# Kernel tuning notes

Hardware: AMD Instinct MI355X
Metric: run time of the kernel (lower is better)

Reference implementation:

```python
import jax, jax.numpy as jnp
import numpy as np
from jax import lax

NUM_HEADS = 8
EPS_BN = 1e-5
EPS_LN = 1e-5


def setup_inputs() -> dict:
    key = jax.random.key(0)
    ks = iter(jax.random.split(key, 32))
    C = 512
    R = C // 16  # channel-gate reduction
    HID = 512    # classifier hidden
    NC = 1       # num_classes

    def gn(shape, scale=0.02):
        return (jax.random.normal(next(ks), shape, dtype=jnp.float32) * scale)

    inp = {
        "x": jax.random.normal(next(ks), (16, C, 28, 28), dtype=jnp.float32),
        # ChannelGate MLP (Linear(C,R) -> ReLU -> Linear(R,C))
        "mlp_w1": gn((R, C)), "mlp_b1": jnp.zeros((R,), jnp.float32),
        "mlp_w2": gn((C, R)), "mlp_b2": jnp.zeros((C,), jnp.float32),
        # SpatialGate 7x7 conv (2->1, no bias) + BatchNorm2d(1) eval-mode stats
        "sp_w": gn((1, 2, 7, 7)),
        "sp_gamma": jnp.ones((1,), jnp.float32), "sp_beta": jnp.zeros((1,), jnp.float32),
        "sp_mean": jnp.zeros((1,), jnp.float32), "sp_var": jnp.ones((1,), jnp.float32),
        # attention projections
        "wq": gn((C, C)), "bq": jnp.zeros((C,), jnp.float32),
        "wk": gn((C, C)), "bk": jnp.zeros((C,), jnp.float32),
        "wv": gn((C, C)), "bv": jnp.zeros((C,), jnp.float32),
        "wo": gn((C, C)), "bo": jnp.zeros((C,), jnp.float32),
        # classifier: LayerNorm(C) -> Linear(C,512) -> ReLU -> Linear(512,NC)
        "ln_g": jnp.ones((C,), jnp.float32), "ln_b": jnp.zeros((C,), jnp.float32),
        "fc1_w": gn((HID, C)), "fc1_b": jnp.zeros((HID,), jnp.float32),
        "fc2_w": gn((NC, HID)), "fc2_b": jnp.zeros((NC,), jnp.float32),
    }
    return inp


def reference(x, mlp_w1, mlp_b1, mlp_w2, mlp_b2, sp_w, sp_gamma, sp_beta,
              sp_mean, sp_var, wq, bq, wk, bk, wv, bv, wo, bo,
              ln_g, ln_b, fc1_w, fc1_b, fc2_w, fc2_b):
    B, C, H, W = x.shape
    N = H * W
    hd = C // NUM_HEADS

    # ---- CBAM: channel gate (avg + max global pools through shared MLP) ----
    def mlp(p):  # p: [B, C]
        return jax.nn.relu(p @ mlp_w1.T + mlp_b1) @ mlp_w2.T + mlp_b2

    avg_p = x.mean(axis=(2, 3))
    max_p = x.max(axis=(2, 3))
    ch_scale = jax.nn.sigmoid(mlp(avg_p) + mlp(max_p))[:, :, None, None]
    x = x * ch_scale

    # ---- CBAM: spatial gate ----
    comp = jnp.concatenate([x.max(axis=1, keepdims=True),
                            x.mean(axis=1, keepdims=True)], axis=1)  # [B,2,H,W]
    s = lax.conv_general_dilated(comp, sp_w, window_strides=(1, 1),
                                 padding=[(3, 3), (3, 3)],
                                 dimension_numbers=("NCHW", "OIHW", "NCHW"))
    s = (s - sp_mean[None, :, None, None]) * lax.rsqrt(sp_var + EPS_BN)[None, :, None, None]
    s = s * sp_gamma[None, :, None, None] + sp_beta[None, :, None, None]
    x = x * jax.nn.sigmoid(s)

    # ---- multi-head self-attention over HW tokens ----
    xf = x.reshape(B, C, N).transpose(0, 2, 1)  # [B, N, C]

    def heads(w, b):
        return (xf @ w.T + b).reshape(B, N, NUM_HEADS, hd).transpose(0, 2, 1, 3)

    Q, K, V = heads(wq, bq), heads(wk, bk), heads(wv, bv)  # [B, h, N, d]
    scores = jnp.einsum("bhnd,bhmd->bhnm", Q, K) / jnp.sqrt(jnp.float32(hd))
    attn = jax.nn.softmax(scores, axis=-1)  # dropout is identity in eval
    attended = jnp.einsum("bhnm,bhmd->bhnd", attn, V)
    attended = attended.transpose(0, 2, 1, 3).reshape(B, N, C)
    attended = attended @ wo.T + bo
    x = x + attended.transpose(0, 2, 1).reshape(B, C, H, W)

    # ---- classifier head ----
    p = x.mean(axis=(2, 3))  # AdaptiveAvgPool2d(1) + Flatten -> [B, C]
    mu = p.mean(axis=-1, keepdims=True)
    var = p.var(axis=-1, keepdims=True)
    ln = (p - mu) * lax.rsqrt(var + EPS_LN) * ln_g + ln_b
    h = jax.nn.relu(ln @ fc1_w.T + fc1_b)
    return h @ fc2_w.T + fc2_b
```

## Files before the change

### kernel.cpp

```cpp
#include <hip/hip_runtime.h>
#include <math.h>

#define BB 16
#define CC 512
#define HW 784
#define RR 32
#define NHD 8
#define HD 64
#define NT 784
#define NTILE 49
#define CBS 132

#define OFS_AVGP   0
#define OFS_MAXP   8192
#define OFS_CHS    16384
#define OFS_SP     49664
#define OFS_P1     62208
#define OFS_ABAR   70400
#define OFS_XG     78592
#define XG_SZ      (BB*CC*HW)
#define OFS_XGT    (OFS_XG + XG_SZ)
#define OFS_QBF    (OFS_XGT + XG_SZ/2)
#define OFS_KBF    (OFS_QBF + XG_SZ/2)
#define OFS_V2     (OFS_KBF + XG_SZ/2)
#define OFS_WF     (OFS_V2 + XG_SZ)
#define OFS_W      OFS_XG
#define OFS_PV     (OFS_XG + 131072)
#define OFS_H1     (OFS_PV + 8192)
#define OFS_CMAXP  (OFS_XG + 262144)
#define OFS_CMEANP (OFS_CMAXP + 200704)

typedef __attribute__((ext_vector_type(8))) short bf16x8;
typedef __attribute__((ext_vector_type(4))) float f32x4;

__device__ __forceinline__ unsigned short f2bf(float x) {
  union { float f; unsigned u; } v; v.f = x;
  unsigned r = v.u + 0x7fffu + ((v.u >> 16) & 1u);
  return (unsigned short)(r >> 16);
}
__device__ __forceinline__ float bf2f(unsigned short x) {
  union { unsigned u; float f; } v; v.u = ((unsigned)x) << 16;
  return v.f;
}
__device__ __forceinline__ void async16(const unsigned short* g, unsigned short* l) {
  __builtin_amdgcn_global_load_lds(
      (const __attribute__((address_space(1))) unsigned int*)g,
      (__attribute__((address_space(3))) unsigned int*)l, 16, 0, 0);
}

__global__ void k_pool(const float* __restrict__ x, float* avg_p, float* max_p) {
  int wid = threadIdx.x >> 6;
  int lane = threadIdx.x & 63;
  int row = blockIdx.x * 4 + wid;
  const float* xr = x + (size_t)row * HW;
  float s = 0.f, m = -INFINITY;
  for (int i = lane; i < HW; i += 64) { float v = xr[i]; s += v; m = fmaxf(m, v); }
  for (int o = 32; o; o >>= 1) { s += __shfl_down(s, o, 64); m = fmaxf(m, __shfl_down(m, o, 64)); }
  if (lane == 0) { avg_p[row] = s * (1.f/HW); max_p[row] = m; }
}

__global__ void k_chmlp(const float* avg_p, const float* max_p,
                        const float* w1, const float* b1,
                        const float* w2, const float* b2, float* chs) {
  __shared__ float pa[CC], pm[CC], part[256], hr[64];
  int b = blockIdx.x, t = threadIdx.x;
  for (int i = t; i < CC; i += 256) { pa[i] = avg_p[b*CC+i]; pm[i] = max_p[b*CC+i]; }
  __syncthreads();
  {
    int rp = t & 63, ch = t >> 6;
    int r = rp & 31;
    const float* src = (rp < 32) ? pa : pm;
    const float* wr = w1 + (size_t)r*CC + ch*128;
    float s = 0.f;
    #pragma unroll 8
    for (int c = 0; c < 128; c++) s += src[ch*128 + c] * wr[c];
    part[t] = s;
  }
  __syncthreads();
  if (t < 64)
    hr[t] = fmaxf(part[t] + part[64+t] + part[128+t] + part[192+t] + b1[t & 31], 0.f);
  __syncthreads();
  for (int c = t; c < CC; c += 256) {
    float a = 2.f*b2[c];
    const float* wr = w2 + c*RR;
    #pragma unroll
    for (int r = 0; r < RR; r++) a += (hr[r]+hr[32+r])*wr[r];
    chs[b*CC+c] = 1.f/(1.f+__expf(-a));
  }
}

__global__ void k_chgatep(const float* __restrict__ x, const float* __restrict__ chs,
                          float* __restrict__ cmaxp, float* __restrict__ cmeanp) {
  __shared__ float cs[32];
  int b = blockIdx.x, cg = blockIdx.y, t = threadIdx.x;
  if (t < 32) cs[t] = chs[b*CC + cg*32 + t];
  __syncthreads();
  const float* xb = x + ((size_t)b*CC + cg*32)*HW;
  for (int pix = t; pix < HW; pix += 256) {
    float mx = -INFINITY, sm = 0.f;
    #pragma unroll
    for (int c = 0; c < 32; c++) {
      float v = xb[(size_t)c*HW + pix] * cs[c];
      mx = fmaxf(mx, v); sm += v;
    }
    cmaxp[(size_t)(cg*BB + b)*HW + pix] = mx;
    cmeanp[(size_t)(cg*BB + b)*HW + pix] = sm;
  }
}

__global__ void k_credsp(const float* __restrict__ cmaxp, const float* __restrict__ cmeanp,
                         const float* __restrict__ w, const float* g, const float* be,
                         const float* mu, const float* var, float* __restrict__ sp) {
  __shared__ float cmx[HW], cmn[HW];
  int b = blockIdx.x, t = threadIdx.x;
  for (int pix = t; pix < HW; pix += 256) {
    float mx = -INFINITY, sm = 0.f;
    #pragma unroll
    for (int cg = 0; cg < 16; cg++) {
      mx = fmaxf(mx, cmaxp[(size_t)(cg*BB + b)*HW + pix]);
      sm += cmeanp[(size_t)(cg*BB + b)*HW + pix];
    }
    cmx[pix] = mx; cmn[pix] = sm * (1.f/CC);
  }
  __syncthreads();
  float bnscale = rsqrtf(var[0]+1e-5f)*g[0];
  for (int pix = t; pix < HW; pix += 256) {
    int h = pix/28, wd = pix%28;
    float acc = 0.f;
    for (int kh = 0; kh < 7; kh++) {
      int ih = h + kh - 3; if (ih < 0 || ih >= 28) continue;
      for (int kw = 0; kw < 7; kw++) {
        int iw = wd + kw - 3; if (iw < 0 || iw >= 28) continue;
        int ip = ih*28+iw;
        acc += cmx[ip]*w[kh*7+kw] + cmn[ip]*w[49+kh*7+kw];
      }
    }
    float s = (acc - mu[0])*bnscale + be[0];
    sp[b*HW+pix] = 1.f/(1.f+__expf(-s));
  }
}

__global__ void k_sfuse(const float* __restrict__ x, const float* __restrict__ chs,
                        const float* __restrict__ sp, unsigned short* __restrict__ xgT) {
  __shared__ float cs[CC];
  int nt = blockIdx.x, b = blockIdx.y;
  int t = threadIdx.x, ln = t & 63;
  for (int i = t; i < CC; i += 256) cs[i] = chs[b*CC+i];
  __syncthreads();
  int n = nt*16 + (ln & 15);
  float spv = sp[b*HW + n];
  const float* xb = x + (size_t)b*CC*HW;
  #pragma unroll
  for (int i = 0; i < 4; i++) {
    int s = (t >> 6) + 4*i;
    int c = s*32 + (ln >> 4)*8;
    bf16x8 p;
    #pragma unroll
    for (int j = 0; j < 8; j++)
      p[j] = (short)f2bf(xb[(size_t)(c+j)*HW + n] * cs[c+j] * spv);
    *(bf16x8*)(xgT + ((((size_t)b*NTILE + nt)*16 + s)*64 + ln)*8) = p;
  }
}

__global__ void k_p1(const unsigned short* __restrict__ xgT, float* __restrict__ p1) {
  __shared__ float red[4][32];
  int b = blockIdx.x, s = blockIdx.y;
  int t = threadIdx.x, w = t >> 6, ln = t & 63;
  float acc[8] = {0.f,0.f,0.f,0.f,0.f,0.f,0.f,0.f};
  for (int nt = w; nt < NTILE; nt += 4) {
    bf16x8 p = *(const bf16x8*)(xgT + ((((size_t)b*NTILE + nt)*16 + s)*64 + ln)*8);
    #pragma unroll
    for (int j = 0; j < 8; j++) acc[j] += bf2f((unsigned short)p[j]);
  }
  #pragma unroll
  for (int j = 0; j < 8; j++) {
    float v = acc[j];
    v += __shfl_xor(v,1,64); v += __shfl_xor(v,2,64);
    v += __shfl_xor(v,4,64); v += __shfl_xor(v,8,64);
    if ((ln & 15) == 0) red[w][(ln>>4)*8 + j] = v;
  }
  __syncthreads();
  if (t < 32)
    p1[b*CC + s*32 + t] = (red[0][t]+red[1][t]+red[2][t]+red[3][t]) * (1.f/HW);
}

__global__ void k_wfrag(const float* __restrict__ wq, const float* __restrict__ wk,
                        const float* __restrict__ wv, unsigned short* __restrict__ Wf) {
  int idx = blockIdx.x*256 + threadIdx.x;
  int ln = idx & 63;
  int s  = (idx >> 6) & 15;
  int ct = (idx >> 10) & 31;
  int mat = idx >> 15;
  const float* W = (mat==0)? wq : (mat==1)? wk : wv;
  const float* src = W + (size_t)(ct*16 + (ln & 15))*CC + s*32 + (ln >> 4)*8;
  float4 f0 = *(const float4*)src;
  float4 f1 = *(const float4*)(src + 4);
  bf16x8 p;
  p[0]=(short)f2bf(f0.x); p[1]=(short)f2bf(f0.y); p[2]=(short)f2bf(f0.z); p[3]=(short)f2bf(f0.w);
  p[4]=(short)f2bf(f1.x); p[5]=(short)f2bf(f1.y); p[6]=(short)f2bf(f1.z); p[7]=(short)f2bf(f1.w);
  *(bf16x8*)(Wf + (size_t)idx*8) = p;
}

__global__ __launch_bounds__(256) void k_qkv_mfma(
    const unsigned short* __restrict__ xgT, const unsigned short* __restrict__ Wf,
    const float* __restrict__ bq, const float* __restrict__ bk, const float* __restrict__ bv,
    unsigned short* __restrict__ Qbf, unsigned short* __restrict__ Kbf,
    unsigned short* __restrict__ Vbf) {
  __shared__ __align__(16) unsigned char smem[65536];
  unsigned short* Alds = (unsigned short*)smem;
  float* Cb = (float*)smem;
  int blk = blockIdx.x;
  int yb = blk / 208;
  int r0 = blk % 208;
  int mt = r0 >> 4;
  int b  = r0 & 15;
  int mat = yb >> 2;
  int c0 = (yb & 3) * 128;
  int t = threadIdx.x, w = t >> 6, ln = t & 63;
  const unsigned short* Ab = xgT + (size_t)b*NTILE*8192;
  const unsigned short* Bb = Wf + (size_t)mat*32*8192;
  int ctg0 = (c0 >> 4) + w*2;
  int ntc[4];
  #pragma unroll
  for (int m = 0; m < 4; m++) { int nt = 4*mt + m; ntc[m] = (nt > 48) ? 48 : nt; }
  #pragma unroll
  for (int j0 = 0; j0 < 16; j0++) {
    int j = w + 4*j0;
    int m = j >> 4, sj = j & 15;
    async16(Ab + (size_t)ntc[m]*8192 + (size_t)(sj*64 + ln)*8,
            Alds + (size_t)j*512);
  }
  f32x4 acc[4][2];
  #pragma unroll
  for (int m = 0; m < 4; m++)
    #pragma unroll
    for (int c2 = 0; c2 < 2; c2++) acc[m][c2] = (f32x4){0.f,0.f,0.f,0.f};
  __syncthreads();
  #pragma unroll 2
  for (int s = 0; s < 16; s++) {
    bf16x8 bf0 = *(const bf16x8*)(Bb + (size_t)(ctg0*16 + s)*512 + ln*8);
    bf16x8 bf1 = *(const bf16x8*)(Bb + (size_t)((ctg0+1)*16 + s)*512 + ln*8);
    bf16x8 af[4];
    #pragma unroll
    for (int m = 0; m < 4; m++)
      af[m] = *(const bf16x8*)(Alds + (size_t)(m*16 + s)*512 + ln*8);
    #pragma unroll
    for (int m = 0; m < 4; m++) {
      acc[m][0] = __builtin_amdgcn_mfma_f32_16x16x32_bf16(af[m], bf0, acc[m][0], 0,0,0);
      acc[m][1] = __builtin_amdgcn_mfma_f32_16x16x32_bf16(af[m], bf1, acc[m][1], 0,0,0);
    }
  }
  __syncthreads();
  #pragma unroll
  for (int m = 0; m < 4; m++)
    #pragma unroll
    for (int c2 = 0; c2 < 2; c2++)
      #pragma unroll
      for (int r = 0; r < 4; r++)
        Cb[(m*16 + (ln>>4)*4 + r)*CBS + w*32 + c2*16 + (ln&15)] = acc[m][c2][r];
  __syncthreads();
  const float* bias = (mat==0)? bq : (mat==1)? bk : bv;
  #pragma unroll
  for (int i = 0; i < 4; i++) {
    int p = w*4 + i;
    int ntl = p >> 2, sl = p & 3;
    int nt = 4*mt + ntl;
    if (nt > 48) continue;
    int row = ntl*16 + (ln & 15);
    int col = sl*32 + (ln >> 4)*8;
    float4 v0 = *(const float4*)&Cb[row*CBS + col];
    float4 v1 = *(const float4*)&Cb[row*CBS + col + 4];
    float v[8] = {v0.x, v0.y, v0.z, v0.w, v1.x, v1.y, v1.z, v1.w};
    #pragma unroll
    for (int j = 0; j < 8; j++) v[j] += bias[c0 + col + j];
    int token = nt*16 + (ln & 15);
    int h = (c0 >> 6) + (sl >> 1);
    int bh = b*NHD + h;
    bf16x8 pk;
    #pragma unroll
    for (int j = 0; j < 8; j++) pk[j] = (short)f2bf(v[j]);
    if (mat < 2) {
      unsigned short* Out = (mat == 0) ? Qbf : Kbf;
      *(bf16x8*)(Out + ((size_t)bh*NTILE + nt)*1024 + (size_t)(sl & 1)*512 + ln*8) = pk;
    } else {
      int d = (sl & 1)*32 + (ln >> 4)*8;
      *(bf16x8*)(Vbf + ((size_t)bh*NT + token)*HD + d) = pk;
    }
  }
}

__global__ __launch_bounds__(256, 3) void k_attn8(const unsigned short* __restrict__ Qbf,
    const unsigned short* __restrict__ Kbf, float* __restrict__ wsum) {
  __shared__ float l_tmp[2][64];
  __shared__ float rl[2][16];
  int bh = blockIdx.x & 127, pg = blockIdx.x >> 7;
  int t = threadIdx.x, w = t >> 6, ln = t & 63;
  int ntA = pg*2;
  bool hasB = (ntA + 1) < NTILE;
  int ntB = hasB ? (ntA + 1) : ntA;
  const unsigned short* QbA = Qbf + ((size_t)bh*NTILE + ntA)*1024;
  const unsigned short* QbB = Qbf + ((size_t)bh*NTILE + ntB)*1024;
  const unsigned short* Kb = Kbf + (size_t)bh*NTILE*1024;
  bf16x8 qA0 = *(const bf16x8*)(QbA + ln*8);
  bf16x8 qA1 = *(const bf16x8*)(QbA + 512 + ln*8);
  bf16x8 qB0 = *(const bf16x8*)(QbB + ln*8);
  bf16x8 qB1 = *(const bf16x8*)(QbB + 512 + ln*8);
  f32x4 evA[13], evB[13];
  float lpA[4] = {0.f,0.f,0.f,0.f}, lpB[4] = {0.f,0.f,0.f,0.f};
  #pragma unroll
  for (int i = 0; i < 13; i++) {
    int mt = w + 4*i;
    bool valid = (i < 12) || (w == 0);
    int mtc = valid ? mt : 48;
    bf16x8 k0 = *(const bf16x8*)(Kb + (size_t)mtc*1024 + ln*8);
    bf16x8 k1 = *(const bf16x8*)(Kb + (size_t)mtc*1024 + 512 + ln*8);
    f32x4 a = {0.f,0.f,0.f,0.f};
    a = __builtin_amdgcn_mfma_f32_16x16x32_bf16(qA0, k0, a, 0,0,0);
    a = __builtin_amdgcn_mfma_f32_16x16x32_bf16(qA1, k1, a, 0,0,0);
    f32x4 c = {0.f,0.f,0.f,0.f};
    c = __builtin_amdgcn_mfma_f32_16x16x32_bf16(qB0, k0, c, 0,0,0);
    c = __builtin_amdgcn_mfma_f32_16x16x32_bf16(qB1, k1, c, 0,0,0);
    f32x4 ea, eb;
    #pragma unroll
    for (int r = 0; r < 4; r++) {
      ea[r] = __expf(a[r]*0.125f);
      eb[r] = __expf(c[r]*0.125f);
    }
    evA[i] = ea; evB[i] = eb;
    if (valid) {
      #pragma unroll
      for (int r = 0; r < 4; r++) { lpA[r] += ea[r]; lpB[r] += eb[r]; }
    }
  }
  #pragma unroll
  for (int r = 0; r < 4; r++) {
    float v = lpA[r];
    v += __shfl_xor(v,1,64); v += __shfl_xor(v,2,64);
    v += __shfl_xor(v,4,64); v += __shfl_xor(v,8,64);
    if ((ln & 15) == 0) l_tmp[0][w*16 + (ln>>4)*4 + r] = v;
    float u = lpB[r];
    u += __shfl_xor(u,1,64); u += __shfl_xor(u,2,64);
    u += __shfl_xor(u,4,64); u += __shfl_xor(u,8,64);
    if ((ln & 15) == 0) l_tmp[1][w*16 + (ln>>4)*4 + r] = u;
  }
  __syncthreads();
  if (t < 32) {
    int g = t >> 4, q = t & 15;
    rl[g][q] = 1.f / (l_tmp[g][q] + l_tmp[g][16+q] + l_tmp[g][32+q] + l_tmp[g][48+q]);
  }
  __syncthreads();
  f32x4 rlA = *(const f32x4*)&rl[0][(ln >> 4)*4];
  f32x4 rlB = *(const f32x4*)&rl[1][(ln >> 4)*4];
  #pragma unroll
  for (int i = 0; i < 13; i++) {
    int mt = w + 4*i;
    bool valid = (i < 12) || (w == 0);
    float v = evA[i][0]*rlA[0] + evA[i][1]*rlA[1] + evA[i][2]*rlA[2] + evA[i][3]*rlA[3];
    if (hasB)
      v += evB[i][0]*rlB[0] + evB[i][1]*rlB[1] + evB[i][2]*rlB[2] + evB[i][3]*rlB[3];
    v += __shfl_xor(v, 16, 64);
    v += __shfl_xor(v, 32, 64);
    if (valid && ln < 16)
      atomicAdd(&wsum[bh*NT + mt*16 + ln], v);
  }
}

__global__ void k_attn_av(const float* __restrict__ w, const unsigned short* __restrict__ Vm,
                          float* __restrict__ abar) {
  __shared__ float red[256];
  int bh = blockIdx.x, t = threadIdx.x;
  int d = t & 63, chunk = t >> 6;
  float acc = 0.f;
  const unsigned short* vb = Vm + (size_t)bh*NT*HD;
  const float* wb = w + bh*NT;
  for (int m = chunk*196; m < (chunk+1)*196; m++)
    acc += wb[m] * bf2f(vb[(size_t)m*HD + d]);
  red[t] = acc;
  __syncthreads();
  if (t < 64)
    abar[bh*HD + t] = (red[t] + red[64+t] + red[128+t] + red[192+t]) * (1.f/NT);
}

__global__ void k_headA(const float* __restrict__ p1, const float* __restrict__ abar,
                        const float* __restrict__ wo, const float* __restrict__ bo,
                        float* __restrict__ pv) {
  int b = blockIdx.x, cg = blockIdx.y;
  int t = threadIdx.x, w = t >> 6, ln = t & 63;
  float a[8];
  #pragma unroll
  for (int k = 0; k < 8; k++) a[k] = abar[b*CC + ln + 64*k];
  int c0 = cg*32 + w*8;
  for (int i = 0; i < 8; i++) {
    int c = c0 + i;
    const float* wr = wo + (size_t)c*CC;
    float s = 0.f;
    #pragma unroll
    for (int k = 0; k < 8; k++) s += a[k] * wr[ln + 64*k];
    for (int o = 32; o; o >>= 1) s += __shfl_down(s, o, 64);
    if (ln == 0) pv[b*CC + c] = s + bo[c] + p1[b*CC + c];
  }
}

__global__ void k_headC(const float* __restrict__ pv, const float* __restrict__ ln_g,
                        const float* __restrict__ ln_b, const float* __restrict__ fc1_w,
                        const float* __restrict__ fc1_b, const float* __restrict__ fc2_w,
                        const float* __restrict__ fc2_b, float* __restrict__ out) {
  int b = blockIdx.x, cg = blockIdx.y;
  int t = threadIdx.x, w = t >> 6, ln = t & 63;
  float a[8];
  float s = 0.f, s2 = 0.f;
  #pragma unroll
  for (int k = 0; k < 8; k++) {
    a[k] = pv[b*CC + ln + 64*k];
    s += a[k]; s2 += a[k]*a[k];
  }
  for (int o = 32; o; o >>= 1) { s += __shfl_down(s, o, 64); s2 += __shfl_down(s2, o, 64); }
  s = __shfl(s, 0, 64); s2 = __shfl(s2, 0, 64);
  float mean = s * (1.f/CC);
  float rs = rsqrtf(s2*(1.f/CC) - mean*mean + 1e-5f);
  #pragma unroll
  for (int k = 0; k < 8; k++)
    a[k] = (a[k]-mean)*rs*ln_g[ln + 64*k] + ln_b[ln + 64*k];
  int c0 = cg*32 + w*8;
  float o2 = 0.f;
  for (int i = 0; i < 8; i++) {
    int c = c0 + i;
    const float* wr = fc1_w + (size_t)c*CC;
    float v = 0.f;
    #pragma unroll
    for (int k = 0; k < 8; k++) v += a[k] * wr[ln + 64*k];
    for (int o = 32; o; o >>= 1) v += __shfl_down(v, o, 64);
    if (ln == 0) o2 += fmaxf(v + fc1_b[c], 0.f) * fc2_w[c];
  }
  if (ln == 0) {
    if (cg == 0 && w == 0) o2 += fc2_b[0];
    atomicAdd(&out[b], o2);
  }
}

extern "C" void kernel_launch(void* const* d_in, const int* in_sizes, int n_in,
                              void* d_out, int out_size, void* d_ws, size_t ws_size,
                              hipStream_t stream) {
  const float* x       = (const float*)d_in[0];
  const float* mlp_w1  = (const float*)d_in[1];
  const float* mlp_b1  = (const float*)d_in[2];
  const float* mlp_w2  = (const float*)d_in[3];
  const float* mlp_b2  = (const float*)d_in[4];
  const float* sp_w    = (const float*)d_in[5];
  const float* sp_g    = (const float*)d_in[6];
  const float* sp_b    = (const float*)d_in[7];
  const float* sp_mu   = (const float*)d_in[8];
  const float* sp_var  = (const float*)d_in[9];
  const float* wq      = (const float*)d_in[10];
  const float* bq      = (const float*)d_in[11];
  const float* wk      = (const float*)d_in[12];
  const float* bk      = (const float*)d_in[13];
  const float* wv      = (const float*)d_in[14];
  const float* bv      = (const float*)d_in[15];
  const float* wo      = (const float*)d_in[16];
  const float* bo      = (const float*)d_in[17];
  const float* ln_g    = (const float*)d_in[18];
  const float* ln_b    = (const float*)d_in[19];
  const float* fc1_w   = (const float*)d_in[20];
  const float* fc1_b   = (const float*)d_in[21];
  const float* fc2_w   = (const float*)d_in[22];
  const float* fc2_b   = (const float*)d_in[23];

  float* ws = (float*)d_ws;
  float* avg_p = ws + OFS_AVGP;
  float* max_p = ws + OFS_MAXP;
  float* chs   = ws + OFS_CHS;
  float* sp    = ws + OFS_SP;
  float* p1    = ws + OFS_P1;
  float* abar  = ws + OFS_ABAR;
  unsigned short* xgT = (unsigned short*)(ws + OFS_XGT);
  unsigned short* Qbf = (unsigned short*)(ws + OFS_QBF);
  unsigned short* Kbf = (unsigned short*)(ws + OFS_KBF);
  unsigned short* Vbf = (unsigned short*)(ws + OFS_V2);
  unsigned short* Wf  = (unsigned short*)(ws + OFS_WF);
  float* wsum  = ws + OFS_W;
  float* pv    = ws + OFS_PV;
  float* cmaxp = ws + OFS_CMAXP;
  float* cmeanp= ws + OFS_CMEANP;

  hipMemsetAsync(wsum, 0, BB*NHD*NT*sizeof(float), stream);
  hipMemsetAsync(d_out, 0, (size_t)out_size*sizeof(float), stream);

  k_pool   <<<2048, 256, 0, stream>>>(x, avg_p, max_p);
  k_chmlp  <<<BB, 256, 0, stream>>>(avg_p, max_p, mlp_w1, mlp_b1, mlp_w2, mlp_b2, chs);
  k_chgatep<<<dim3(BB,16), 256, 0, stream>>>(x, chs, cmaxp, cmeanp);
  k_credsp <<<BB, 256, 0, stream>>>(cmaxp, cmeanp, sp_w, sp_g, sp_b, sp_mu, sp_var, sp);
  k_wfrag  <<<384, 256, 0, stream>>>(wq, wk, wv, Wf);
  k_sfuse  <<<dim3(NTILE,BB), 256, 0, stream>>>(x, chs, sp, xgT);
  k_p1     <<<dim3(BB,16), 256, 0, stream>>>(xgT, p1);
  k_qkv_mfma<<<2496, 256, 0, stream>>>(xgT, Wf, bq, bk, bv, Qbf, Kbf, Vbf);
  k_attn8  <<<25*128, 256, 0, stream>>>(Qbf, Kbf, wsum);
  k_attn_av<<<128, 256, 0, stream>>>(wsum, Vbf, abar);
  k_headA  <<<dim3(BB,16), 256, 0, stream>>>(p1, abar, wo, bo, pv);
  k_headC  <<<dim3(BB,16), 256, 0, stream>>>(pv, ln_g, ln_b, fc1_w, fc1_b,
                                             fc2_w, fc2_b, (float*)d_out);
}
```

Before: 270.5 us.

## Fuse prologue, pooling and head kernels; widen QKV tile to 256 columns

Merges the pooling, weight-fragment conversion and workspace zeroing into one launch, which removes the two memsets. The p1 channel mean is folded into the spatial-fuse kernel via shuffle reductions and atomics, computed from fp32 values instead of rereading the bf16 output. The attention-average, output projection, LayerNorm and classifier are fused into a single 512-thread kernel per batch. The QKV MFMA kernel now computes 256 columns per block, halving its grid and reusing each A tile more. The spatial conv is split across four blocks per batch. This cuts launch count and global round trips, at the cost of a very small, serial head kernel (16 blocks) and more float atomics.

Measured after the change: 350.2 us. +29.5%, slower.

```diff
diff --git a/kernel.cpp b/kernel.cpp
--- a/kernel.cpp
+++ b/kernel.cpp
@@ -25,8 +25,6 @@
 #define OFS_V2     (OFS_KBF + XG_SZ/2)
 #define OFS_WF     (OFS_V2 + XG_SZ)
 #define OFS_W      OFS_XG
-#define OFS_PV     (OFS_XG + 131072)
-#define OFS_H1     (OFS_PV + 8192)
 #define OFS_CMAXP  (OFS_XG + 262144)
 #define OFS_CMEANP (OFS_CMAXP + 200704)
 
@@ -48,15 +46,43 @@
       (__attribute__((address_space(3))) unsigned int*)l, 16, 0, 0);
 }
 
-__global__ void k_pool(const float* __restrict__ x, float* avg_p, float* max_p) {
-  int wid = threadIdx.x >> 6;
-  int lane = threadIdx.x & 63;
-  int row = blockIdx.x * 4 + wid;
-  const float* xr = x + (size_t)row * HW;
-  float s = 0.f, m = -INFINITY;
-  for (int i = lane; i < HW; i += 64) { float v = xr[i]; s += v; m = fmaxf(m, v); }
-  for (int o = 32; o; o >>= 1) { s += __shfl_down(s, o, 64); m = fmaxf(m, __shfl_down(m, o, 64)); }
-  if (lane == 0) { avg_p[row] = s * (1.f/HW); max_p[row] = m; }
+__global__ void k_pre(const float* __restrict__ x,
+                      const float* __restrict__ wq, const float* __restrict__ wk,
+                      const float* __restrict__ wv,
+                      float* avg_p, float* max_p, unsigned short* __restrict__ Wf,
+                      float* __restrict__ wsum, float* __restrict__ p1) {
+  int bid = blockIdx.x;
+  if (bid < 2048) {
+    int wid = threadIdx.x >> 6;
+    int lane = threadIdx.x & 63;
+    int row = bid * 4 + wid;
+    const float* xr = x + (size_t)row * HW;
+    float s = 0.f, m = -INFINITY;
+    for (int i = lane; i < HW; i += 64) { float v = xr[i]; s += v; m = fmaxf(m, v); }
+    for (int o = 32; o; o >>= 1) { s += __shfl_down(s, o, 64); m = fmaxf(m, __shfl_down(m, o, 64)); }
+    if (lane == 0) { avg_p[row] = s * (1.f/HW); max_p[row] = m; }
+  } else if (bid < 2432) {
+    int idx = (bid - 2048)*256 + threadIdx.x;
+    int ln = idx & 63;
+    int s  = (idx >> 6) & 15;
+    int ct = (idx >> 10) & 31;
+    int mat = idx >> 15;
+    const float* W = (mat==0)? wq : (mat==1)? wk : wv;
+    const float* src = W + (size_t)(ct*16 + (ln & 15))*CC + s*32 + (ln >> 4)*8;
+    float4 f0 = *(const float4*)src;
+    float4 f1 = *(const float4*)(src + 4);
+    bf16x8 p;
+    p[0]=(short)f2bf(f0.x); p[1]=(short)f2bf(f0.y); p[2]=(short)f2bf(f0.z); p[3]=(short)f2bf(f0.w);
+    p[4]=(short)f2bf(f1.x); p[5]=(short)f2bf(f1.y); p[6]=(short)f2bf(f1.z); p[7]=(short)f2bf(f1.w);
+    *(bf16x8*)(Wf + (size_t)idx*8) = p;
+  } else {
+    int idx = (bid - 2432)*256 + threadIdx.x;
+    const float4 z = {0.f,0.f,0.f,0.f};
+    for (int i = idx; i < 27136; i += 16384) {
+      if (i < 25088) *(float4*)&wsum[(size_t)i*4] = z;
+      else           *(float4*)&p1[(size_t)(i-25088)*4] = z;
+    }
+  }
 }
 
 __global__ void k_chmlp(const float* avg_p, const float* max_p,
@@ -112,7 +138,7 @@
                          const float* __restrict__ w, const float* g, const float* be,
                          const float* mu, const float* var, float* __restrict__ sp) {
   __shared__ float cmx[HW], cmn[HW];
-  int b = blockIdx.x, t = threadIdx.x;
+  int b = blockIdx.x, q = blockIdx.y, t = threadIdx.x;
   for (int pix = t; pix < HW; pix += 256) {
     float mx = -INFINITY, sm = 0.f;
     #pragma unroll
@@ -123,8 +149,9 @@
     cmx[pix] = mx; cmn[pix] = sm * (1.f/CC);
   }
   __syncthreads();
-  float bnscale = rsqrtf(var[0]+1e-5f)*g[0];
-  for (int pix = t; pix < HW; pix += 256) {
+  if (t < 196) {
+    int pix = q*196 + t;
+    float bnscale = rsqrtf(var[0]+1e-5f)*g[0];
     int h = pix/28, wd = pix%28;
     float acc = 0.f;
     for (int kh = 0; kh < 7; kh++) {
@@ -141,7 +168,8 @@
 }
 
 __global__ void k_sfuse(const float* __restrict__ x, const float* __restrict__ chs,
-                        const float* __restrict__ sp, unsigned short* __restrict__ xgT) {
+                        const float* __restrict__ sp, unsigned short* __restrict__ xgT,
+                        float* __restrict__ p1) {
   __shared__ float cs[CC];
   int nt = blockIdx.x, b = blockIdx.y;
   int t = threadIdx.x, ln = t & 63;
@@ -154,51 +182,26 @@
   for (int i = 0; i < 4; i++) {
     int s = (t >> 6) + 4*i;
     int c = s*32 + (ln >> 4)*8;
+    float vf[8];
     bf16x8 p;
     #pragma unroll
-    for (int j = 0; j < 8; j++)
-      p[j] = (short)f2bf(xb[(size_t)(c+j)*HW + n] * cs[c+j] * spv);
+    for (int j = 0; j < 8; j++) {
+      vf[j] = xb[(size_t)(c+j)*HW + n] * cs[c+j] * spv;
+      p[j] = (short)f2bf(vf[j]);
+    }
     *(bf16x8*)(xgT + ((((size_t)b*NTILE + nt)*16 + s)*64 + ln)*8) = p;
-  }
-}
-
-__global__ void k_p1(const unsigned short* __restrict__ xgT, float* __restrict__ p1) {
-  __shared__ float red[4][32];
-  int b = blockIdx.x, s = blockIdx.y;
-  int t = threadIdx.x, w = t >> 6, ln = t & 63;
-  float acc[8] = {0.f,0.f,0.f,0.f,0.f,0.f,0.f,0.f};
-  for (int nt = w; nt < NTILE; nt += 4) {
-    bf16x8 p = *(const bf16x8*)(xgT + ((((size_t)b*NTILE + nt)*16 + s)*64 + ln)*8);
-    #pragma unroll
-    for (int j = 0; j < 8; j++) acc[j] += bf2f((unsigned short)p[j]);
-  }
-  #pragma unroll
-  for (int j = 0; j < 8; j++) {
-    float v = acc[j];
-    v += __shfl_xor(v,1,64); v += __shfl_xor(v,2,64);
-    v += __shfl_xor(v,4,64); v += __shfl_xor(v,8,64);
-    if ((ln & 15) == 0) red[w][(ln>>4)*8 + j] = v;
-  }
-  __syncthreads();
-  if (t < 32)
-    p1[b*CC + s*32 + t] = (red[0][t]+red[1][t]+red[2][t]+red[3][t]) * (1.f/HW);
-}
-
-__global__ void k_wfrag(const float* __restrict__ wq, const float* __restrict__ wk,
-                        const float* __restrict__ wv, unsigned short* __restrict__ Wf) {
-  int idx = blockIdx.x*256 + threadIdx.x;
-  int ln = idx & 63;
-  int s  = (idx >> 6) & 15;
-  int ct = (idx >> 10) & 31;
-  int mat = idx >> 15;
-  const float* W = (mat==0)? wq : (mat==1)? wk : wv;
-  const float* src = W + (size_t)(ct*16 + (ln & 15))*CC + s*32 + (ln >> 4)*8;
-  float4 f0 = *(const float4*)src;
-  float4 f1 = *(const float4*)(src + 4);
-  bf16x8 p;
-  p[0]=(short)f2bf(f0.x); p[1]=(short)f2bf(f0.y); p[2]=(short)f2bf(f0.z); p[3]=(short)f2bf(f0.w);
-  p[4]=(short)f2bf(f1.x); p[5]=(short)f2bf(f1.y); p[6]=(short)f2bf(f1.z); p[7]=(short)f2bf(f1.w);
-  *(bf16x8*)(Wf + (size_t)idx*8) = p;
+    #pragma unroll
+    for (int j = 0; j < 8; j++) {
+      float v = vf[j];
+      v += __shfl_xor(v,1,64); v += __shfl_xor(v,2,64);
+      v += __shfl_xor(v,4,64); v += __shfl_xor(v,8,64);
+      vf[j] = v;
+    }
+    if ((ln & 15) == 0) {
+      #pragma unroll
+      for (int j = 0; j < 8; j++) atomicAdd(&p1[b*CC + c + j], vf[j]);
+    }
+  }
 }
 
 __global__ __launch_bounds__(256) void k_qkv_mfma(
@@ -214,12 +217,12 @@
   int r0 = blk % 208;
   int mt = r0 >> 4;
   int b  = r0 & 15;
-  int mat = yb >> 2;
-  int c0 = (yb & 3) * 128;
+  int mat = yb >> 1;
+  int c0 = (yb & 1) * 256;
   int t = threadIdx.x, w = t >> 6, ln = t & 63;
   const unsigned short* Ab = xgT + (size_t)b*NTILE*8192;
   const unsigned short* Bb = Wf + (size_t)mat*32*8192;
-  int ctg0 = (c0 >> 4) + w*2;
+  int ctgb = (c0 >> 4) + w*2;
   int ntc[4];
   #pragma unroll
   for (int m = 0; m < 4; m++) { int nt = 4*mt + m; ntc[m] = (nt > 48) ? 48 : nt; }
@@ -230,61 +233,70 @@
     async16(Ab + (size_t)ntc[m]*8192 + (size_t)(sj*64 + ln)*8,
             Alds + (size_t)j*512);
   }
-  f32x4 acc[4][2];
+  f32x4 acc[4][4];
   #pragma unroll
   for (int m = 0; m < 4; m++)
     #pragma unroll
-    for (int c2 = 0; c2 < 2; c2++) acc[m][c2] = (f32x4){0.f,0.f,0.f,0.f};
+    for (int c2 = 0; c2 < 4; c2++) acc[m][c2] = (f32x4){0.f,0.f,0.f,0.f};
   __syncthreads();
   #pragma unroll 2
   for (int s = 0; s < 16; s++) {
-    bf16x8 bf0 = *(const bf16x8*)(Bb + (size_t)(ctg0*16 + s)*512 + ln*8);
-    bf16x8 bf1 = *(const bf16x8*)(Bb + (size_t)((ctg0+1)*16 + s)*512 + ln*8);
+    bf16x8 bf[4];
+    bf[0] = *(const bf16x8*)(Bb + (size_t)((ctgb  )*16 + s)*512 + ln*8);
+    bf[1] = *(const bf16x8*)(Bb + (size_t)((ctgb+1)*16 + s)*512 + ln*8);
+    bf[2] = *(const bf16x8*)(Bb + (size_t)((ctgb+8)*16 + s)*512 + ln*8);
+    bf[3] = *(const bf16x8*)(Bb + (size_t)((ctgb+9)*16 + s)*512 + ln*8);
     bf16x8 af[4];
     #pragma unroll
     for (int m = 0; m < 4; m++)
       af[m] = *(const bf16x8*)(Alds + (size_t)(m*16 + s)*512 + ln*8);
     #pragma unroll
     for (int m = 0; m < 4; m++) {
-      acc[m][0] = __builtin_amdgcn_mfma_f32_16x16x32_bf16(af[m], bf0, acc[m][0], 0,0,0);
-      acc[m][1] = __builtin_amdgcn_mfma_f32_16x16x32_bf16(af[m], bf1, acc[m][1], 0,0,0);
-    }
-  }
-  __syncthreads();
-  #pragma unroll
-  for (int m = 0; m < 4; m++)
-    #pragma unroll
-    for (int c2 = 0; c2 < 2; c2++)
-      #pragma unroll
-      for (int r = 0; r < 4; r++)
-        Cb[(m*16 + (ln>>4)*4 + r)*CBS + w*32 + c2*16 + (ln&15)] = acc[m][c2][r];
+      #pragma unroll
+      for (int c2 = 0; c2 < 4; c2++)
+        acc[m][c2] = __builtin_amdgcn_mfma_f32_16x16x32_bf16(af[m], bf[c2], acc[m][c2], 0,0,0);
+    }
+  }
   __syncthreads();
   const float* bias = (mat==0)? bq : (mat==1)? bk : bv;
   #pragma unroll
-  for (int i = 0; i < 4; i++) {
-    int p = w*4 + i;
-    int ntl = p >> 2, sl = p & 3;
-    int nt = 4*mt + ntl;
-    if (nt > 48) continue;
-    int row = ntl*16 + (ln & 15);
-    int col = sl*32 + (ln >> 4)*8;
-    float4 v0 = *(const float4*)&Cb[row*CBS + col];
-    float4 v1 = *(const float4*)&Cb[row*CBS + col + 4];
-    float v[8] = {v0.x, v0.y, v0.z, v0.w, v1.x, v1.y, v1.z, v1.w};
-    #pragma unroll
-    for (int j = 0; j < 8; j++) v[j] += bias[c0 + col + j];
-    int token = nt*16 + (ln & 15);
-    int h = (c0 >> 6) + (sl >> 1);
-    int bh = b*NHD + h;
-    bf16x8 pk;
-    #pragma unroll
-    for (int j = 0; j < 8; j++) pk[j] = (short)f2bf(v[j]);
-    if (mat < 2) {
-      unsigned short* Out = (mat == 0) ? Qbf : Kbf;
-      *(bf16x8*)(Out + ((size_t)bh*NTILE + nt)*1024 + (size_t)(sl & 1)*512 + ln*8) = pk;
-    } else {
-      int d = (sl & 1)*32 + (ln >> 4)*8;
-      *(bf16x8*)(Vbf + ((size_t)bh*NT + token)*HD + d) = pk;
+  for (int ch = 0; ch < 2; ch++) {
+    if (ch) __syncthreads();
+    #pragma unroll
+    for (int m = 0; m < 4; m++)
+      #pragma unroll
+      for (int c2 = 0; c2 < 2; c2++)
+        #pragma unroll
+        for (int r = 0; r < 4; r++)
+          Cb[(m*16 + (ln>>4)*4 + r)*CBS + w*32 + c2*16 + (ln&15)] = acc[m][ch*2+c2][r];
+    __syncthreads();
+    #pragma unroll
+    for (int i = 0; i < 4; i++) {
+      int p = w*4 + i;
+      int ntl = p >> 2, sl = p & 3;
+      int nt = 4*mt + ntl;
+      if (nt > 48) continue;
+      int row = ntl*16 + (ln & 15);
+      int col = sl*32 + (ln >> 4)*8;
+      float4 v0 = *(const float4*)&Cb[row*CBS + col];
+      float4 v1 = *(const float4*)&Cb[row*CBS + col + 4];
+      float v[8] = {v0.x, v0.y, v0.z, v0.w, v1.x, v1.y, v1.z, v1.w};
+      int colA = ch*128 + col;
+      #pragma unroll
+      for (int j = 0; j < 8; j++) v[j] += bias[c0 + colA + j];
+      int token = nt*16 + (ln & 15);
+      int h = (c0 >> 6) + (ch << 1) + (sl >> 1);
+      int bh = b*NHD + h;
+      bf16x8 pk;
+      #pragma unroll
+      for (int j = 0; j < 8; j++) pk[j] = (short)f2bf(v[j]);
+      if (mat < 2) {
+        unsigned short* Out = (mat == 0) ? Qbf : Kbf;
+        *(bf16x8*)(Out + ((size_t)bh*NTILE + nt)*1024 + (size_t)(sl & 1)*512 + ln*8) = pk;
+      } else {
+        int d = (sl & 1)*32 + (ln >> 4)*8;
+        *(bf16x8*)(Vbf + ((size_t)bh*NT + token)*HD + d) = pk;
+      }
     }
   }
 }
@@ -365,76 +377,81 @@
   }
 }
 
-__global__ void k_attn_av(const float* __restrict__ w, const unsigned short* __restrict__ Vm,
-                          float* __restrict__ abar) {
-  __shared__ float red[256];
-  int bh = blockIdx.x, t = threadIdx.x;
-  int d = t & 63, chunk = t >> 6;
-  float acc = 0.f;
-  const unsigned short* vb = Vm + (size_t)bh*NT*HD;
-  const float* wb = w + bh*NT;
-  for (int m = chunk*196; m < (chunk+1)*196; m++)
-    acc += wb[m] * bf2f(vb[(size_t)m*HD + d]);
-  red[t] = acc;
-  __syncthreads();
-  if (t < 64)
-    abar[bh*HD + t] = (red[t] + red[64+t] + red[128+t] + red[192+t]) * (1.f/NT);
-}
-
-__global__ void k_headA(const float* __restrict__ p1, const float* __restrict__ abar,
-                        const float* __restrict__ wo, const float* __restrict__ bo,
-                        float* __restrict__ pv) {
-  int b = blockIdx.x, cg = blockIdx.y;
-  int t = threadIdx.x, w = t >> 6, ln = t & 63;
-  float a[8];
-  #pragma unroll
-  for (int k = 0; k < 8; k++) a[k] = abar[b*CC + ln + 64*k];
-  int c0 = cg*32 + w*8;
-  for (int i = 0; i < 8; i++) {
-    int c = c0 + i;
-    const float* wr = wo + (size_t)c*CC;
-    float s = 0.f;
-    #pragma unroll
-    for (int k = 0; k < 8; k++) s += a[k] * wr[ln + 64*k];
-    for (int o = 32; o; o >>= 1) s += __shfl_down(s, o, 64);
-    if (ln == 0) pv[b*CC + c] = s + bo[c] + p1[b*CC + c];
-  }
-}
-
-__global__ void k_headC(const float* __restrict__ pv, const float* __restrict__ ln_g,
-                        const float* __restrict__ ln_b, const float* __restrict__ fc1_w,
-                        const float* __restrict__ fc1_b, const float* __restrict__ fc2_w,
-                        const float* __restrict__ fc2_b, float* __restrict__ out) {
-  int b = blockIdx.x, cg = blockIdx.y;
-  int t = threadIdx.x, w = t >> 6, ln = t & 63;
-  float a[8];
-  float s = 0.f, s2 = 0.f;
-  #pragma unroll
-  for (int k = 0; k < 8; k++) {
-    a[k] = pv[b*CC + ln + 64*k];
-    s += a[k]; s2 += a[k]*a[k];
-  }
-  for (int o = 32; o; o >>= 1) { s += __shfl_down(s, o, 64); s2 += __shfl_down(s2, o, 64); }
-  s = __shfl(s, 0, 64); s2 = __shfl(s2, 0, 64);
-  float mean = s * (1.f/CC);
-  float rs = rsqrtf(s2*(1.f/CC) - mean*mean + 1e-5f);
-  #pragma unroll
-  for (int k = 0; k < 8; k++)
-    a[k] = (a[k]-mean)*rs*ln_g[ln + 64*k] + ln_b[ln + 64*k];
-  int c0 = cg*32 + w*8;
-  float o2 = 0.f;
-  for (int i = 0; i < 8; i++) {
-    int c = c0 + i;
-    const float* wr = fc1_w + (size_t)c*CC;
-    float v = 0.f;
-    #pragma unroll
-    for (int k = 0; k < 8; k++) v += a[k] * wr[ln + 64*k];
-    for (int o = 32; o; o >>= 1) v += __shfl_down(v, o, 64);
-    if (ln == 0) o2 += fmaxf(v + fc1_b[c], 0.f) * fc2_w[c];
-  }
-  if (ln == 0) {
-    if (cg == 0 && w == 0) o2 += fc2_b[0];
-    atomicAdd(&out[b], o2);
+__global__ __launch_bounds__(512) void k_head(const float* __restrict__ wsum,
+    const unsigned short* __restrict__ Vbf, const float* __restrict__ p1,
+    const float* __restrict__ wo, const float* __restrict__ bo,
+    const float* __restrict__ ln_g, const float* __restrict__ ln_b,
+    const float* __restrict__ fc1_w, const float* __restrict__ fc1_b,
+    const float* __restrict__ fc2_w, const float* __restrict__ fc2_b,
+    float* __restrict__ out) {
+  __shared__ float abar_s[CC];
+  __shared__ float pv_s[CC];
+  __shared__ float aln[CC];
+  __shared__ float red2[16];
+  __shared__ float osum[8];
+  int b = blockIdx.x, t = threadIdx.x, w = t >> 6, ln = t & 63;
+  {
+    const unsigned short* vb = Vbf + (size_t)(b*NHD + w)*NT*HD;
+    const float* wb = wsum + (b*NHD + w)*NT;
+    float a0 = 0.f, a1 = 0.f, a2 = 0.f, a3 = 0.f;
+    for (int m = 0; m < NT; m += 4) {
+      a0 += wb[m]   * bf2f(vb[(size_t)m*HD + ln]);
+      a1 += wb[m+1] * bf2f(vb[(size_t)(m+1)*HD + ln]);
+      a2 += wb[m+2] * bf2f(vb[(size_t)(m+2)*HD + ln]);
+      a3 += wb[m+3] * bf2f(vb[(size_t)(m+3)*HD + ln]);
+    }
+    abar_s[w*HD + ln] = (a0+a1+a2+a3) * (1.f/NT);
+  }
+  __syncthreads();
+  {
+    float a[8];
+    #pragma unroll
+    for (int k = 0; k < 8; k++) a[k] = abar_s[ln + 64*k];
+    for (int i = 0; i < 64; i++) {
+      int c = w*64 + i;
+      const float* wr = wo + (size_t)c*CC;
+      float s = 0.f;
+      #pragma unroll
+      for (int k = 0; k < 8; k++) s += a[k] * wr[ln + 64*k];
+      for (int o = 32; o; o >>= 1) s += __shfl_down(s, o, 64);
+      if (ln == 0) pv_s[c] = s + bo[c] + p1[b*CC + c] * (1.f/HW);
+    }
+  }
+  __syncthreads();
+  float v = pv_s[t];
+  float s1 = v, s2 = v*v;
+  for (int o = 32; o; o >>= 1) { s1 += __shfl_down(s1,o,64); s2 += __shfl_down(s2,o,64); }
+  if (ln == 0) { red2[w] = s1; red2[8+w] = s2; }
+  __syncthreads();
+  float S1 = 0.f, S2 = 0.f;
+  #pragma unroll
+  for (int k = 0; k < 8; k++) { S1 += red2[k]; S2 += red2[8+k]; }
+  float mean = S1 * (1.f/CC);
+  float rs = rsqrtf(S2*(1.f/CC) - mean*mean + 1e-5f);
+  aln[t] = (v - mean)*rs*ln_g[t] + ln_b[t];
+  __syncthreads();
+  {
+    float a[8];
+    #pragma unroll
+    for (int k = 0; k < 8; k++) a[k] = aln[ln + 64*k];
+    float o2 = 0.f;
+    for (int i = 0; i < 64; i++) {
+      int h = w*64 + i;
+      const float* wr = fc1_w + (size_t)h*CC;
+      float s = 0.f;
+      #pragma unroll
+      for (int k = 0; k < 8; k++) s += a[k] * wr[ln + 64*k];
+      for (int o = 32; o; o >>= 1) s += __shfl_down(s, o, 64);
+      if (ln == 0) o2 += fmaxf(s + fc1_b[h], 0.f) * fc2_w[h];
+    }
+    if (ln == 0) osum[w] = o2;
+  }
+  __syncthreads();
+  if (t == 0) {
+    float r = fc2_b[0];
+    #pragma unroll
+    for (int k = 0; k < 8; k++) r += osum[k];
+    out[b] = r;
   }
 }
 
@@ -472,31 +489,22 @@
   float* chs   = ws + OFS_CHS;
   float* sp    = ws + OFS_SP;
   float* p1    = ws + OFS_P1;
-  float* abar  = ws + OFS_ABAR;
   unsigned short* xgT = (unsigned short*)(ws + OFS_XGT);
   unsigned short* Qbf = (unsigned short*)(ws + OFS_QBF);
   unsigned short* Kbf = (unsigned short*)(ws + OFS_KBF);
   unsigned short* Vbf = (unsigned short*)(ws + OFS_V2);
   unsigned short* Wf  = (unsigned short*)(ws + OFS_WF);
   float* wsum  = ws + OFS_W;
-  float* pv    = ws + OFS_PV;
   float* cmaxp = ws + OFS_CMAXP;
   float* cmeanp= ws + OFS_CMEANP;
 
-  hipMemsetAsync(wsum, 0, BB*NHD*NT*sizeof(float), stream);
-  hipMemsetAsync(d_out, 0, (size_t)out_size*sizeof(float), stream);
-
-  k_pool   <<<2048, 256, 0, stream>>>(x, avg_p, max_p);
+  k_pre    <<<2496, 256, 0, stream>>>(x, wq, wk, wv, avg_p, max_p, Wf, wsum, p1);
   k_chmlp  <<<BB, 256, 0, stream>>>(avg_p, max_p, mlp_w1, mlp_b1, mlp_w2, mlp_b2, chs);
   k_chgatep<<<dim3(BB,16), 256, 0, stream>>>(x, chs, cmaxp, cmeanp);
-  k_credsp <<<BB, 256, 0, stream>>>(cmaxp, cmeanp, sp_w, sp_g, sp_b, sp_mu, sp_var, sp);
-  k_wfrag  <<<384, 256, 0, stream>>>(wq, wk, wv, Wf);
-  k_sfuse  <<<dim3(NTILE,BB), 256, 0, stream>>>(x, chs, sp, xgT);
-  k_p1     <<<dim3(BB,16), 256, 0, stream>>>(xgT, p1);
-  k_qkv_mfma<<<2496, 256, 0, stream>>>(xgT, Wf, bq, bk, bv, Qbf, Kbf, Vbf);
+  k_credsp <<<dim3(BB,4), 256, 0, stream>>>(cmaxp, cmeanp, sp_w, sp_g, sp_b, sp_mu, sp_var, sp);
+  k_sfuse  <<<dim3(NTILE,BB), 256, 0, stream>>>(x, chs, sp, xgT, p1);
+  k_qkv_mfma<<<1248, 256, 0, stream>>>(xgT, Wf, bq, bk, bv, Qbf, Kbf, Vbf);
   k_attn8  <<<25*128, 256, 0, stream>>>(Qbf, Kbf, wsum);
-  k_attn_av<<<128, 256, 0, stream>>>(wsum, Vbf, abar);
-  k_headA  <<<dim3(BB,16), 256, 0, stream>>>(p1, abar, wo, bo, pv);
-  k_headC  <<<dim3(BB,16), 256, 0, stream>>>(pv, ln_g, ln_b, fc1_w, fc1_b,
-                                             fc2_w, fc2_b, (float*)d_out);
-}
+  k_head   <<<BB, 512, 0, stream>>>(wsum, Vbf, p1, wo, bo, ln_g, ln_b,
+                                    fc1_w, fc1_b, fc2_w, fc2_b, (float*)d_out);
+}
```
